# Performance work log

Hardware: AMD Instinct MI355X
Metric: run time of the kernel (lower is better)

Reference implementation:

```python
import jax, jax.numpy as jnp
import numpy as np
from jax import lax

RADII = (0.1, 0.2, 0.4)
NSAMPLES = (16, 32, 128)
MLPS = ((3, 32, 32, 64), (3, 64, 64, 128), (3, 64, 96, 128))  # divide_ratio=1


def fps(xyz, npoint):
    # iterative farthest point sampling; xyz [B,N,3] -> idx [B,npoint]
    B, N, _ = xyz.shape
    def body(carry, _):
        mind, last = carry
        p = jnp.take_along_axis(xyz, last[:, None, None], axis=1)  # [B,1,3]
        d = jnp.sum((xyz - p) ** 2, -1)
        mind = jnp.minimum(mind, d)
        nxt = jnp.argmax(mind, -1).astype(jnp.int32)
        return (mind, nxt), last
    init = (jnp.full((B, N), 1e10, xyz.dtype), jnp.zeros((B,), jnp.int32))
    _, idx = lax.scan(body, init, None, length=npoint)
    return jnp.transpose(idx)  # [B,npoint]


def ball_query(radius, nsample, xyz, new_xyz):
    # first-nsample neighbors within radius; pad with first valid index
    N = xyz.shape[1]
    sq = jnp.sum((new_xyz[:, :, None, :] - xyz[:, None, :, :]) ** 2, -1)  # [B,S,N]
    cand = jnp.where(sq < radius * radius,
                     jnp.arange(N, dtype=jnp.int32)[None, None, :], N)
    idx = jnp.sort(cand, axis=-1)[:, :, :nsample]
    first = idx[:, :, :1]
    return jnp.where(idx == N, first, idx).astype(jnp.int32)


def scale_branch(xyz, new_xyz, radius, nsample, weights):
    idx = ball_query(radius, nsample, xyz, new_xyz)
    grouped = jax.vmap(lambda x, i: x[i])(xyz, idx)          # [B,S,ns,3]
    h = grouped - new_xyz[:, :, None, :]                      # relative coords (points=None)
    for w, b in weights:                                      # shared 1x1-conv MLP
        h = jax.nn.relu(jnp.einsum('bsnc,co->bsno', h, w) + b)
    return jnp.max(h, axis=2)                                 # maxpool over neighbors [B,S,C]


def _forward(pcd, params, wf, bf):
    npoint = pcd.shape[1] // 8
    idx = fps(pcd, npoint)
    new_xyz = jnp.take_along_axis(pcd, idx[:, :, None], axis=1)  # [B,S,3]
    feats = [scale_branch(pcd, new_xyz, RADII[i], NSAMPLES[i], params[i]) for i in range(3)]
    h = jnp.concatenate(feats, axis=-1)                          # [B,S,320]
    return jnp.einsum('bsc,co->bso', h, wf) + bf                 # patch values [B,S,1]


def setup_inputs() -> dict:
    key = jax.random.key(0)
    ks = jax.random.split(key, 32)
    B, N = 8, 4096
    inp = {"pcd": jax.random.uniform(ks[0], (B, N, 3), jnp.float32)}
    ki = 1
    for si, dims in enumerate(MLPS):
        for li in range(3):
            cin, cout = dims[li], dims[li + 1]
            inp[f"w{si}{li}"] = jax.random.normal(ks[ki], (cin, cout), jnp.float32) * (2.0 / cin) ** 0.5
            inp[f"b{si}{li}"] = jnp.zeros((cout,), jnp.float32)
            ki += 1
    inp["wf"] = jax.random.normal(ks[ki], (320, 1), jnp.float32) * 0.05
    inp["bf"] = jnp.zeros((1,), jnp.float32)
    return inp


def reference(pcd, w00, b00, w01, b01, w02, b02,
              w10, b10, w11, b11, w12, b12,
              w20, b20, w21, b21, w22, b22, wf, bf):
    params = [[(w00, b00), (w01, b01), (w02, b02)],
              [(w10, b10), (w11, b11), (w12, b12)],
              [(w20, b20), (w21, b21), (w22, b22)]]
    return _forward(pcd, params, wf, bf)
```

## Files before the change

kernel.cpp:

```cpp
#include <hip/hip_runtime.h>

#define BATCH 8
#define NPTS 4096
#define NSAMP 512

#define ROW_SHR(n) (0x110 | (n))
#define ROW_BCAST15 0x142
#define ROW_BCAST31 0x143

template <int CTRL, int RMASK>
__device__ __forceinline__ float fmax_dpp(float x) {
  int t = __builtin_amdgcn_update_dpp(0, __float_as_int(x), CTRL, RMASK, 0xf, true);
  return fmaxf(x, __int_as_float(t));
}

__device__ __forceinline__ float wave_max(float x) {
  x = fmax_dpp<ROW_SHR(1), 0xf>(x);
  x = fmax_dpp<ROW_SHR(2), 0xf>(x);
  x = fmax_dpp<ROW_SHR(4), 0xf>(x);
  x = fmax_dpp<ROW_SHR(8), 0xf>(x);
  x = fmax_dpp<ROW_BCAST15, 0xa>(x);
  x = fmax_dpp<ROW_BCAST31, 0xc>(x);
  return x;
}

__device__ __forceinline__ void tsec(int g, const float* __restrict__ w,
                                     float* __restrict__ wt, int cin, int cinp,
                                     int cout, int base) {
  int local = g - base;
  if (local < 0 || local >= cinp * cout) return;
  int oc = local / cinp, ic = local % cinp;
  wt[base + local] = (ic < cin) ? w[ic * cout + oc] : 0.0f;
}

#define W00 0
#define W01 128
#define W02 1152
#define W10 3200
#define W11 3456
#define W12 7552
#define WT_TOTAL 15744

__global__ __launch_bounds__(256) void prep_kernel(
    const float* w00, const float* w01, const float* w02,
    const float* w10, const float* w11, const float* w12,
    float* __restrict__ wt) {
  int g = blockIdx.x * 256 + threadIdx.x;
  tsec(g, w00, wt, 3, 4, 32, W00);
  tsec(g, w01, wt, 32, 32, 32, W01);
  tsec(g, w02, wt, 32, 32, 64, W02);
  tsec(g, w10, wt, 3, 4, 64, W10);
  tsec(g, w11, wt, 64, 64, 64, W11);
  tsec(g, w12, wt, 64, 64, 128, W12);
}

template <int TOC, int TN>
__device__ __forceinline__ void ib(float (&acc)[TOC][TN], const float* bias) {
#pragma unroll
  for (int j = 0; j < TOC; ++j) {
    float bj = bias[j];
#pragma unroll
    for (int i = 0; i < TN; ++i) acc[j][i] = bj;
  }
}

template <int CIN4, int TOC, int TN, int NTPI, int WS>
__device__ __forceinline__ void layer_acc(const float* __restrict__ wtb,
                                          const float* hin,
                                          float (&acc)[TOC][TN], int tn) {
#pragma unroll 2
  for (int c4 = 0; c4 < CIN4; ++c4) {
    float hv[4][TN];
#pragma unroll
    for (int k = 0; k < 4; ++k) {
      const float* src = &hin[(c4 * 4 + k) * NTPI + tn * TN];
      if constexpr (TN == 1) {
        hv[k][0] = src[0];
      } else if constexpr (TN == 2) {
        float2 v = *(const float2*)src; hv[k][0] = v.x; hv[k][1] = v.y;
      } else {
        float4 v = *(const float4*)src;
        hv[k][0] = v.x; hv[k][1] = v.y; hv[k][2] = v.z; hv[k][3] = v.w;
      }
    }
#pragma unroll
    for (int j = 0; j < TOC; ++j) {
      float4 w4 = *(const float4*)&wtb[j * WS + c4 * 4];
#pragma unroll
      for (int i = 0; i < TN; ++i) {
        acc[j][i] = fmaf(hv[0][i], w4.x, acc[j][i]);
        acc[j][i] = fmaf(hv[1][i], w4.y, acc[j][i]);
        acc[j][i] = fmaf(hv[2][i], w4.z, acc[j][i]);
        acc[j][i] = fmaf(hv[3][i], w4.w, acc[j][i]);
      }
    }
  }
}

template <int TOC, int TN, int NTPO>
__device__ __forceinline__ void store_relu(float* hout,
                                           float (&acc)[TOC][TN], int tn) {
#pragma unroll
  for (int j = 0; j < TOC; ++j) {
    float* dst = &hout[j * NTPO + tn * TN];
    if constexpr (TN == 1) {
      dst[0] = fmaxf(acc[j][0], 0.0f);
    } else if constexpr (TN == 2) {
      *(float2*)dst = make_float2(fmaxf(acc[j][0], 0.0f),
                                  fmaxf(acc[j][1], 0.0f));
    } else {
      *(float4*)dst = make_float4(fmaxf(acc[j][0], 0.0f),
                                  fmaxf(acc[j][1], 0.0f),
                                  fmaxf(acc[j][2], 0.0f),
                                  fmaxf(acc[j][3], 0.0f));
    }
  }
}

template <int TOC, int TN>
__device__ __forceinline__ float rmax_dot(const float* wfp,
                                          float (&acc)[TOC][TN], int tn) {
  float s = 0.0f;
#pragma unroll
  for (int j = 0; j < TOC; ++j) {
    float v = 0.0f;
#pragma unroll
    for (int i = 0; i < TN; ++i) v = fmaxf(v, acc[j][i]);
    v = fmaxf(v, __shfl_xor(v, 1));
    v = fmaxf(v, __shfl_xor(v, 2));
    v = fmaxf(v, __shfl_xor(v, 4));
    v = fmaxf(v, __shfl_xor(v, 8));
    if (tn == 0) s = fmaf(v, wfp[j], s);
  }
  return s;
}

__global__ __launch_bounds__(256) void fused_kernel(
    const float* __restrict__ pcd, float* __restrict__ new_xyz,
    int* __restrict__ ctrl, const float* __restrict__ wt,
    const float* __restrict__ w20o, const float* __restrict__ w21o,
    const float* __restrict__ w22o,
    const float* __restrict__ b00, const float* __restrict__ b01,
    const float* __restrict__ b02, const float* __restrict__ b10,
    const float* __restrict__ b11, const float* __restrict__ b12,
    const float* __restrict__ b20, const float* __restrict__ b21,
    const float* __restrict__ b22,
    const float* __restrict__ wf, const float* __restrict__ bf,
    float* __restrict__ out) {
  __shared__ __align__(16) float lds[10240];

  const int tid = threadIdx.x;
  int* progress = ctrl + 8;

  if (tid == 0) ((int*)lds)[0] = atomicAdd(&ctrl[0], 1);
  __syncthreads();
  const int ticket = ((int*)lds)[0];

  if (ticket < BATCH) {
    const int b = ticket;
    const int t = tid;
    const int wave = t >> 6, lane = t & 63;
    const float* xb = pcd + (size_t)b * NPTS * 3;
    float4* slot = (float4*)(lds + 16);

    float X[16], Y[16], Z[16], mind[16];
    {
      float f[48];
      float4* vv = (float4*)f;
      const float4* src = (const float4*)xb + t * 12;
#pragma unroll
      for (int q = 0; q < 12; ++q) vv[q] = src[q];
#pragma unroll
      for (int j = 0; j < 16; ++j) {
        X[j] = f[3 * j + 0]; Y[j] = f[3 * j + 1]; Z[j] = f[3 * j + 2];
        mind[j] = 10000000000.0f;
      }
    }
    float px = xb[0], py = xb[1], pz = xb[2];

    for (int it = 0; it < NSAMP; ++it) {
      if (t == 0) {
        int* dst = (int*)(new_xyz + ((size_t)b * NSAMP + it) * 3);
        atomicExch(&dst[0], __float_as_int(px));
        atomicExch(&dst[1], __float_as_int(py));
        atomicExch(&dst[2], __float_as_int(pz));
        if ((it & 7) == 7)
          __hip_atomic_store(&progress[b], it + 1, __ATOMIC_RELEASE,
                             __HIP_MEMORY_SCOPE_AGENT);
      }
      float bv = -1.0f, bx = 0.0f, by = 0.0f, bz = 0.0f;
#pragma unroll
      for (int j = 0; j < 16; ++j) {
        float dx = __fsub_rn(X[j], px);
        float dy = __fsub_rn(Y[j], py);
        float dz = __fsub_rn(Z[j], pz);
        float d = __fadd_rn(__fadd_rn(__fmul_rn(dx, dx), __fmul_rn(dy, dy)),
                            __fmul_rn(dz, dz));
        float m = fminf(mind[j], d);
        mind[j] = m;
        bool g = m > bv;
        bv = g ? m : bv;
        bx = g ? X[j] : bx; by = g ? Y[j] : by; bz = g ? Z[j] : bz;
      }
      float wmax = __int_as_float(
          __builtin_amdgcn_readlane(__float_as_int(wave_max(bv)), 63));
      unsigned long long msk = __ballot(bv == wmax);
      if (lane == __ffsll(msk) - 1)
        slot[(it & 1) * 4 + wave] = make_float4(bx, by, bz, wmax);
      __syncthreads();
      float4 cur = slot[(it & 1) * 4 + 0];
#pragma unroll
      for (int w = 1; w < 4; ++w) {
        float4 sw = slot[(it & 1) * 4 + w];
        if (sw.w > cur.w) cur = sw;
      }
      px = cur.x; py = cur.y; pz = cur.z;
    }
    return;
  }

  const int tk = ticket - BATCH;
  const int b = tk & 7;
  const int s = tk >> 3;
  const int bs = (b << 9) | s;
  const int lane = tid & 63;
  const int wave = tid >> 6;
  const int tn = tid & 15, toc = tid >> 4;
  const float* xb = pcd + (size_t)b * NPTS * 3;

  float* h1 = lds;
  float* h2 = lds + 4096;
  float* sB = lds + 4096;
  float* sA = lds + 6272;
  float* cbuf = lds + 8448;
  unsigned short* gl = (unsigned short*)(lds + 8720);
  float* bc = lds + 4;
  float* wsum = lds + 8;
  unsigned long long* masks = (unsigned long long*)(lds + 64);

  if (tid == 0) {
    while (__hip_atomic_load(&progress[b], __ATOMIC_ACQUIRE,
                             __HIP_MEMORY_SCOPE_AGENT) <= s)
      __builtin_amdgcn_s_sleep(2);
    const int* src = (const int*)(new_xyz + (size_t)bs * 3);
    bc[0] = __int_as_float(__hip_atomic_load(&src[0], __ATOMIC_RELAXED,
                                             __HIP_MEMORY_SCOPE_AGENT));
    bc[1] = __int_as_float(__hip_atomic_load(&src[1], __ATOMIC_RELAXED,
                                             __HIP_MEMORY_SCOPE_AGENT));
    bc[2] = __int_as_float(__hip_atomic_load(&src[2], __ATOMIC_RELAXED,
                                             __HIP_MEMORY_SCOPE_AGENT));
  }
  __syncthreads();
  const float cx = bc[0], cy = bc[1], cz = bc[2];

  const float r2a = (float)(0.1 * 0.1);
  const float r2b = (float)(0.2 * 0.2);
  const float r2c = (float)(0.4 * 0.4);
#pragma unroll 4
  for (int j = 0; j < 16; ++j) {
    int i = (j << 8) | tid;
    const float* p = xb + i * 3;
    float dx = __fsub_rn(cx, p[0]);
    float dy = __fsub_rn(cy, p[1]);
    float dz = __fsub_rn(cz, p[2]);
    float sq = __fadd_rn(__fadd_rn(__fmul_rn(dx, dx), __fmul_rn(dy, dy)),
                         __fmul_rn(dz, dz));
    unsigned long long m0 = __ballot(sq < r2a);
    unsigned long long m1 = __ballot(sq < r2b);
    unsigned long long m2 = __ballot(sq < r2c);
    if (lane == 0) {
      int c = (j << 2) | wave;
      masks[0 * 64 + c] = m0; masks[1 * 64 + c] = m1; masks[2 * 64 + c] = m2;
    }
  }
  __syncthreads();

  if (wave < 3) {
    const int ns  = (wave == 0) ? 16 : (wave == 1) ? 32 : 128;
    const int off = (wave == 0) ? 0  : (wave == 1) ? 16 : 48;
    unsigned long long m = masks[wave * 64 + lane];
    int pc = (int)__popcll(m);
    int incl = pc;
#pragma unroll
    for (int o = 1; o < 64; o <<= 1) {
      int u = __shfl_up(incl, o);
      if (lane >= o) incl += u;
    }
    int ex = incl - pc;
    int total = __shfl(incl, 63);
    unsigned short* glw = gl + off;
    unsigned long long mm = m;
    int p = ex;
    while (mm && p < ns) {
      int l = (int)__builtin_ctzll(mm);
      mm &= mm - 1;
      glw[p++] = (unsigned short)((lane << 6) | l);
    }
    int cnt = total < ns ? total : ns;
    unsigned long long nz = __ballot(pc > 0);
    int fl = __ffsll(nz) - 1;
    int myf = (lane << 6) | (int)__builtin_ctzll(m | 0x8000000000000000ull);
    int fidx = __shfl(myf, fl);
    for (int k = cnt + lane; k < ns; k += 64) glw[k] = (unsigned short)fidx;
  }
  __syncthreads();

  if (tid < 68) cbuf[3 * 68 + tid] = 0.0f;
  if (tid < 48) {
    int j = gl[tid];
    const float* p = xb + 3 * j;
    cbuf[0 * 68 + tid] = __fsub_rn(p[0], cx);
    cbuf[1 * 68 + tid] = __fsub_rn(p[1], cy);
    cbuf[2 * 68 + tid] = __fsub_rn(p[2], cz);
  }
  const int gi0 = gl[48 + lane];
  const int gi1 = gl[112 + lane];
  __syncthreads();

  const int wq = __builtin_amdgcn_readfirstlane(wave);
  float dot = 0.0f;

  {
    float a[2][1]; ib<2, 1>(a, b00 + toc * 2);
    layer_acc<1, 2, 1, 68, 4>(wt + W00 + (toc * 2) * 4, cbuf, a, tn);
    store_relu<2, 1, 18>(sB + (toc * 2) * 18, a, tn);
  }
  __syncthreads();

  {
    float a[2][1]; ib<2, 1>(a, b01 + toc * 2);
    layer_acc<8, 2, 1, 18, 32>(wt + W01 + (toc * 2) * 32, sB, a, tn);
    store_relu<2, 1, 18>(sA + (toc * 2) * 18, a, tn);
  }
  __syncthreads();

  {
    float a[4][1]; ib<4, 1>(a, b02 + toc * 4);
    layer_acc<8, 4, 1, 18, 32>(wt + W02 + (toc * 4) * 32, sA, a, tn);
    dot += rmax_dot<4, 1>(wf + toc * 4, a, tn);
    float a1[4][2]; ib<4, 2>(a1, b10 + toc * 4);
    layer_acc<1, 4, 2, 68, 4>(wt + W10 + (toc * 4) * 4, cbuf + 16, a1, tn);
    store_relu<4, 2, 34>(sB + (toc * 4) * 34, a1, tn);
  }
  __syncthreads();

  {
    float a[4][2]; ib<4, 2>(a, b11 + toc * 4);
    layer_acc<16, 4, 2, 34, 64>(wt + W11 + (toc * 4) * 64, sB, a, tn);
    store_relu<4, 2, 34>(sA + (toc * 4) * 34, a, tn);
  }
  __syncthreads();

  {
    float a[8][2]; ib<8, 2>(a, b12 + toc * 8);
    layer_acc<16, 8, 2, 34, 64>(wt + W12 + (toc * 8) * 64, sA, a, tn);
    dot += rmax_dot<8, 2>(wf + 64 + toc * 8, a, tn);
    const float* p = xb + 3 * gi0;
    float dx = __fsub_rn(p[0], cx);
    float dy = __fsub_rn(p[1], cy);
    float dz = __fsub_rn(p[2], cz);
    const float* wp = w20o + wq * 16;
    const float* bp = b20 + wq * 16;
#pragma unroll
    for (int j = 0; j < 16; ++j) {
      float a2 = bp[j];
      a2 = fmaf(dx, wp[0 * 64 + j], a2);
      a2 = fmaf(dy, wp[1 * 64 + j], a2);
      a2 = fmaf(dz, wp[2 * 64 + j], a2);
      h1[(wq * 16 + j) * 64 + lane] = fmaxf(a2, 0.0f);
    }
  }
  __syncthreads();

  float rm2[32];
#pragma unroll
  for (int j = 0; j < 32; ++j) rm2[j] = 0.0f;

  {
    const float* wp = w21o + wq * 24;
    const float* bp = b21 + wq * 24;
    float acc[24];
#pragma unroll
    for (int j = 0; j < 24; ++j) acc[j] = bp[j];
#pragma unroll 4
    for (int k = 0; k < 64; ++k) {
      float hv = h1[k * 64 + lane];
#pragma unroll
      for (int j = 0; j < 24; ++j) acc[j] = fmaf(hv, wp[k * 96 + j], acc[j]);
    }
#pragma unroll
    for (int j = 0; j < 24; ++j)
      h2[(wq * 24 + j) * 64 + lane] = fmaxf(acc[j], 0.0f);
  }
  __syncthreads();

  {
    const float* p = xb + 3 * gi1;
    float dx = __fsub_rn(p[0], cx);
    float dy = __fsub_rn(p[1], cy);
    float dz = __fsub_rn(p[2], cz);
    const float* wp0 = w20o + wq * 16;
    const float* bp0 = b20 + wq * 16;
#pragma unroll
    for (int j = 0; j < 16; ++j) {
      float a2 = bp0[j];
      a2 = fmaf(dx, wp0[0 * 64 + j], a2);
      a2 = fmaf(dy, wp0[1 * 64 + j], a2);
      a2 = fmaf(dz, wp0[2 * 64 + j], a2);
      h1[(wq * 16 + j) * 64 + lane] = fmaxf(a2, 0.0f);
    }
    const float* wp = w22o + wq * 32;
    const float* bp = b22 + wq * 32;
    float acc[32];
#pragma unroll
    for (int j = 0; j < 32; ++j) acc[j] = bp[j];
#pragma unroll 2
    for (int k = 0; k < 96; ++k) {
      float hv = h2[k * 64 + lane];
#pragma unroll
      for (int j = 0; j < 32; ++j) acc[j] = fmaf(hv, wp[k * 128 + j], acc[j]);
    }
#pragma unroll
    for (int j = 0; j < 32; ++j) rm2[j] = fmaxf(rm2[j], fmaxf(acc[j], 0.0f));
  }
  __syncthreads();

  {
    const float* wp = w21o + wq * 24;
    const float* bp = b21 + wq * 24;
    float acc[24];
#pragma unroll
    for (int j = 0; j < 24; ++j) acc[j] = bp[j];
#pragma unroll 4
    for (int k = 0; k < 64; ++k) {
      float hv = h1[k * 64 + lane];
#pragma unroll
      for (int j = 0; j < 24; ++j) acc[j] = fmaf(hv, wp[k * 96 + j], acc[j]);
    }
#pragma unroll
    for (int j = 0; j < 24; ++j)
      h2[(wq * 24 + j) * 64 + lane] = fmaxf(acc[j], 0.0f);
  }
  __syncthreads();

  {
    const float* wp = w22o + wq * 32;
    const float* bp = b22 + wq * 32;
    float acc[32];
#pragma unroll
    for (int j = 0; j < 32; ++j) acc[j] = bp[j];
#pragma unroll 2
    for (int k = 0; k < 96; ++k) {
      float hv = h2[k * 64 + lane];
#pragma unroll
      for (int j = 0; j < 32; ++j) acc[j] = fmaf(hv, wp[k * 128 + j], acc[j]);
    }
#pragma unroll
    for (int j = 0; j < 32; ++j) {
      float v = fmaxf(rm2[j], fmaxf(acc[j], 0.0f));
      v = wave_max(v);
      if (lane == 63) dot = fmaf(v, wf[192 + wq * 32 + j], dot);
    }
  }

#pragma unroll
  for (int o = 1; o < 64; o <<= 1) dot += __shfl_xor(dot, o);
  if (lane == 0) wsum[wq] = dot;
  __syncthreads();
  if (tid == 0)
    out[bs] = wsum[0] + wsum[1] + wsum[2] + wsum[3] + bf[0];
}

extern "C" void kernel_launch(void* const* d_in, const int* in_sizes, int n_in,
                              void* d_out, int out_size, void* d_ws, size_t ws_size,
                              hipStream_t stream) {
  const float* pcd = (const float*)d_in[0];
  float* wsf = (float*)d_ws;
  float* new_xyz = wsf;
  float* wt = wsf + 12288;
  int* ctrl = (int*)(wsf + 28288);

  hipMemsetAsync(ctrl, 0, 64, stream);

  prep_kernel<<<(WT_TOTAL + 255) / 256, 256, 0, stream>>>(
      (const float*)d_in[1], (const float*)d_in[3], (const float*)d_in[5],
      (const float*)d_in[7], (const float*)d_in[9], (const float*)d_in[11],
      wt);

  fused_kernel<<<BATCH * NSAMP + BATCH, 256, 0, stream>>>(
      pcd, new_xyz, ctrl, wt,
      (const float*)d_in[13], (const float*)d_in[15], (const float*)d_in[17],
      (const float*)d_in[2],  (const float*)d_in[4],  (const float*)d_in[6],
      (const float*)d_in[8],  (const float*)d_in[10], (const float*)d_in[12],
      (const float*)d_in[14], (const float*)d_in[16], (const float*)d_in[18],
      (const float*)d_in[19], (const float*)d_in[20],
      (float*)d_out);
}
```

Before: 510.9 us.

## Fuse scale-2 first MLP layer into second layer and repack weights

The third-scale branch no longer writes its first-layer activations (h1) to LDS. Each thread now recomputes the 3-input layer per k on the fly, inside the second-layer loop, reading weights from a row-packed buffer that holds w20, b20 and a w21 slice contiguously. The w22 weights are also repacked per wave into contiguous 32-wide slices, and the LDS footprint shrinks from 10240 to 6160 floats, which may raise occupancy. The cost is extra FMAs per k, a larger prep kernel, and a bigger workspace.

```diff
diff --git a/kernel.cpp b/kernel.cpp
--- a/kernel.cpp
+++ b/kernel.cpp
@@ -33,17 +33,47 @@
   wt[base + local] = (ic < cin) ? w[ic * cout + oc] : 0.0f;
 }
 
+__device__ __forceinline__ void rowpack(int g, const float* __restrict__ w20,
+                                        const float* __restrict__ b20,
+                                        const float* __restrict__ w21,
+                                        float* __restrict__ wt, int base) {
+  int local = g - base;
+  if (local < 0 || local >= 4 * 64 * 32) return;
+  int wq = local / (64 * 32);
+  int r = local % (64 * 32);
+  int k = r / 32, j = r % 32;
+  float v;
+  if (j < 3) v = w20[j * 64 + k];
+  else if (j == 3) v = b20[k];
+  else if (j < 28) v = w21[k * 96 + wq * 24 + (j - 4)];
+  else v = 0.0f;
+  wt[base + local] = v;
+}
+
+__device__ __forceinline__ void wsec22(int g, const float* __restrict__ w,
+                                       float* __restrict__ wt, int base) {
+  int local = g - base;
+  if (local < 0 || local >= 4 * 96 * 32) return;
+  int wq = local / (96 * 32);
+  int r = local % (96 * 32);
+  int k = r / 32, j = r % 32;
+  wt[base + local] = w[k * 128 + wq * 32 + j];
+}
+
 #define W00 0
 #define W01 128
 #define W02 1152
 #define W10 3200
 #define W11 3456
 #define W12 7552
-#define WT_TOTAL 15744
+#define WROW 15744
+#define W22T 23936
+#define WT_TOTAL 36224
 
 __global__ __launch_bounds__(256) void prep_kernel(
     const float* w00, const float* w01, const float* w02,
     const float* w10, const float* w11, const float* w12,
+    const float* w20, const float* b20, const float* w21, const float* w22,
     float* __restrict__ wt) {
   int g = blockIdx.x * 256 + threadIdx.x;
   tsec(g, w00, wt, 3, 4, 32, W00);
@@ -52,6 +82,8 @@
   tsec(g, w10, wt, 3, 4, 64, W10);
   tsec(g, w11, wt, 64, 64, 64, W11);
   tsec(g, w12, wt, 64, 64, 128, W12);
+  rowpack(g, w20, b20, w21, wt, WROW);
+  wsec22(g, w22, wt, W22T);
 }
 
 template <int TOC, int TN>
@@ -138,16 +170,13 @@
 __global__ __launch_bounds__(256) void fused_kernel(
     const float* __restrict__ pcd, float* __restrict__ new_xyz,
     int* __restrict__ ctrl, const float* __restrict__ wt,
-    const float* __restrict__ w20o, const float* __restrict__ w21o,
-    const float* __restrict__ w22o,
     const float* __restrict__ b00, const float* __restrict__ b01,
     const float* __restrict__ b02, const float* __restrict__ b10,
     const float* __restrict__ b11, const float* __restrict__ b12,
-    const float* __restrict__ b20, const float* __restrict__ b21,
-    const float* __restrict__ b22,
+    const float* __restrict__ b21, const float* __restrict__ b22,
     const float* __restrict__ wf, const float* __restrict__ bf,
     float* __restrict__ out) {
-  __shared__ __align__(16) float lds[10240];
+  __shared__ __align__(16) float lds[6160];
 
   const int tid = threadIdx.x;
   int* progress = ctrl + 8;
@@ -228,15 +257,14 @@
   const int tn = tid & 15, toc = tid >> 4;
   const float* xb = pcd + (size_t)b * NPTS * 3;
 
-  float* h1 = lds;
-  float* h2 = lds + 4096;
-  float* sB = lds + 4096;
-  float* sA = lds + 6272;
-  float* cbuf = lds + 8448;
-  unsigned short* gl = (unsigned short*)(lds + 8720);
   float* bc = lds + 4;
   float* wsum = lds + 8;
-  unsigned long long* masks = (unsigned long long*)(lds + 64);
+  float* h2 = lds + 16;
+  unsigned long long* masks = (unsigned long long*)(lds + 16);
+  unsigned short* gl = (unsigned short*)(lds + 400);
+  float* cbuf = lds + 488;
+  float* sB = lds + 760;
+  float* sA = lds + 2936;
 
   if (tid == 0) {
     while (__hip_atomic_load(&progress[b], __ATOMIC_ACQUIRE,
@@ -305,6 +333,8 @@
   }
   __syncthreads();
 
+  const int gi0 = gl[48 + lane];
+  const int gi1 = gl[112 + lane];
   if (tid < 68) cbuf[3 * 68 + tid] = 0.0f;
   if (tid < 48) {
     int j = gl[tid];
@@ -313,8 +343,14 @@
     cbuf[1 * 68 + tid] = __fsub_rn(p[1], cy);
     cbuf[2 * 68 + tid] = __fsub_rn(p[2], cz);
   }
-  const int gi0 = gl[48 + lane];
-  const int gi1 = gl[112 + lane];
+  const float* q0 = xb + 3 * gi0;
+  const float* q1 = xb + 3 * gi1;
+  const float dx0 = __fsub_rn(q0[0], cx);
+  const float dy0 = __fsub_rn(q0[1], cy);
+  const float dz0 = __fsub_rn(q0[2], cz);
+  const float dx1 = __fsub_rn(q1[0], cx);
+  const float dy1 = __fsub_rn(q1[1], cy);
+  const float dz1 = __fsub_rn(q1[2], cz);
   __syncthreads();
 
   const int wq = __builtin_amdgcn_readfirstlane(wave);
@@ -355,20 +391,6 @@
     float a[8][2]; ib<8, 2>(a, b12 + toc * 8);
     layer_acc<16, 8, 2, 34, 64>(wt + W12 + (toc * 8) * 64, sA, a, tn);
     dot += rmax_dot<8, 2>(wf + 64 + toc * 8, a, tn);
-    const float* p = xb + 3 * gi0;
-    float dx = __fsub_rn(p[0], cx);
-    float dy = __fsub_rn(p[1], cy);
-    float dz = __fsub_rn(p[2], cz);
-    const float* wp = w20o + wq * 16;
-    const float* bp = b20 + wq * 16;
-#pragma unroll
-    for (int j = 0; j < 16; ++j) {
-      float a2 = bp[j];
-      a2 = fmaf(dx, wp[0 * 64 + j], a2);
-      a2 = fmaf(dy, wp[1 * 64 + j], a2);
-      a2 = fmaf(dz, wp[2 * 64 + j], a2);
-      h1[(wq * 16 + j) * 64 + lane] = fmaxf(a2, 0.0f);
-    }
   }
   __syncthreads();
 
@@ -377,16 +399,21 @@
   for (int j = 0; j < 32; ++j) rm2[j] = 0.0f;
 
   {
-    const float* wp = w21o + wq * 24;
+    const float* wp = wt + WROW + wq * 2048;
     const float* bp = b21 + wq * 24;
     float acc[24];
 #pragma unroll
     for (int j = 0; j < 24; ++j) acc[j] = bp[j];
 #pragma unroll 4
     for (int k = 0; k < 64; ++k) {
-      float hv = h1[k * 64 + lane];
-#pragma unroll
-      for (int j = 0; j < 24; ++j) acc[j] = fmaf(hv, wp[k * 96 + j], acc[j]);
+      const float* row = wp + k * 32;
+      float a2 = row[3];
+      a2 = fmaf(dx0, row[0], a2);
+      a2 = fmaf(dy0, row[1], a2);
+      a2 = fmaf(dz0, row[2], a2);
+      float hv = fmaxf(a2, 0.0f);
+#pragma unroll
+      for (int j = 0; j < 24; ++j) acc[j] = fmaf(hv, row[4 + j], acc[j]);
     }
 #pragma unroll
     for (int j = 0; j < 24; ++j)
@@ -395,21 +422,7 @@
   __syncthreads();
 
   {
-    const float* p = xb + 3 * gi1;
-    float dx = __fsub_rn(p[0], cx);
-    float dy = __fsub_rn(p[1], cy);
-    float dz = __fsub_rn(p[2], cz);
-    const float* wp0 = w20o + wq * 16;
-    const float* bp0 = b20 + wq * 16;
-#pragma unroll
-    for (int j = 0; j < 16; ++j) {
-      float a2 = bp0[j];
-      a2 = fmaf(dx, wp0[0 * 64 + j], a2);
-      a2 = fmaf(dy, wp0[1 * 64 + j], a2);
-      a2 = fmaf(dz, wp0[2 * 64 + j], a2);
-      h1[(wq * 16 + j) * 64 + lane] = fmaxf(a2, 0.0f);
-    }
-    const float* wp = w22o + wq * 32;
+    const float* wp = wt + W22T + wq * 3072;
     const float* bp = b22 + wq * 32;
     float acc[32];
 #pragma unroll
@@ -418,7 +431,7 @@
     for (int k = 0; k < 96; ++k) {
       float hv = h2[k * 64 + lane];
 #pragma unroll
-      for (int j = 0; j < 32; ++j) acc[j] = fmaf(hv, wp[k * 128 + j], acc[j]);
+      for (int j = 0; j < 32; ++j) acc[j] = fmaf(hv, wp[k * 32 + j], acc[j]);
     }
 #pragma unroll
     for (int j = 0; j < 32; ++j) rm2[j] = fmaxf(rm2[j], fmaxf(acc[j], 0.0f));
@@ -426,16 +439,21 @@
   __syncthreads();
 
   {
-    const float* wp = w21o + wq * 24;
+    const float* wp = wt + WROW + wq * 2048;
     const float* bp = b21 + wq * 24;
     float acc[24];
 #pragma unroll
     for (int j = 0; j < 24; ++j) acc[j] = bp[j];
 #pragma unroll 4
     for (int k = 0; k < 64; ++k) {
-      float hv = h1[k * 64 + lane];
-#pragma unroll
-      for (int j = 0; j < 24; ++j) acc[j] = fmaf(hv, wp[k * 96 + j], acc[j]);
+      const float* row = wp + k * 32;
+      float a2 = row[3];
+      a2 = fmaf(dx1, row[0], a2);
+      a2 = fmaf(dy1, row[1], a2);
+      a2 = fmaf(dz1, row[2], a2);
+      float hv = fmaxf(a2, 0.0f);
+#pragma unroll
+      for (int j = 0; j < 24; ++j) acc[j] = fmaf(hv, row[4 + j], acc[j]);
     }
 #pragma unroll
     for (int j = 0; j < 24; ++j)
@@ -444,7 +462,7 @@
   __syncthreads();
 
   {
-    const float* wp = w22o + wq * 32;
+    const float* wp = wt + W22T + wq * 3072;
     const float* bp = b22 + wq * 32;
     float acc[32];
 #pragma unroll
@@ -453,7 +471,7 @@
     for (int k = 0; k < 96; ++k) {
       float hv = h2[k * 64 + lane];
 #pragma unroll
-      for (int j = 0; j < 32; ++j) acc[j] = fmaf(hv, wp[k * 128 + j], acc[j]);
+      for (int j = 0; j < 32; ++j) acc[j] = fmaf(hv, wp[k * 32 + j], acc[j]);
     }
 #pragma unroll
     for (int j = 0; j < 32; ++j) {
@@ -478,21 +496,21 @@
   float* wsf = (float*)d_ws;
   float* new_xyz = wsf;
   float* wt = wsf + 12288;
-  int* ctrl = (int*)(wsf + 28288);
+  int* ctrl = (int*)(wsf + 48512);
 
   hipMemsetAsync(ctrl, 0, 64, stream);
 
   prep_kernel<<<(WT_TOTAL + 255) / 256, 256, 0, stream>>>(
       (const float*)d_in[1], (const float*)d_in[3], (const float*)d_in[5],
       (const float*)d_in[7], (const float*)d_in[9], (const float*)d_in[11],
-      wt);
+      (const float*)d_in[13], (const float*)d_in[14], (const float*)d_in[15],
+      (const float*)d_in[17], wt);
 
   fused_kernel<<<BATCH * NSAMP + BATCH, 256, 0, stream>>>(
       pcd, new_xyz, ctrl, wt,
-      (const float*)d_in[13], (const float*)d_in[15], (const float*)d_in[17],
       (const float*)d_in[2],  (const float*)d_in[4],  (const float*)d_in[6],
       (const float*)d_in[8],  (const float*)d_in[10], (const float*)d_in[12],
-      (const float*)d_in[14], (const float*)d_in[16], (const float*)d_in[18],
+      (const float*)d_in[16], (const float*)d_in[18],
       (const float*)d_in[19], (const float*)d_in[20],
       (float*)d_out);
 }
```

New measurement: 530.3 us. +3.8%, slower.
